# Kernel optimization log

Hardware: AMD Instinct MI355X
Metric: run time of the kernel (lower is better)

## Reference

```python
import jax, jax.numpy as jnp
import numpy as np

N, EMB, ATT = 65536, 1024, 512


def setup_inputs() -> dict:
    key = jax.random.key(0)
    k = jax.random.split(key, 6)
    scale = 0.02
    return {
        "leaves": jax.random.normal(k[0], (N, EMB), dtype=jnp.float32),
        "ancestors": jax.random.normal(k[1], (N, EMB), dtype=jnp.float32),
        "W1": jax.random.normal(k[2], (2 * EMB, ATT), dtype=jnp.float32) * scale,
        "b1": jax.random.normal(k[3], (ATT,), dtype=jnp.float32) * scale,
        "W2": jax.random.normal(k[4], (ATT, 1), dtype=jnp.float32) * scale,
        "b2": jax.random.normal(k[5], (1,), dtype=jnp.float32) * scale,
    }


def reference(leaves, ancestors, W1, b1, W2, b2):
    # concat -> [N, 2*EMB]
    x = jnp.concatenate([leaves, ancestors], axis=-1)
    # additive attention MLP: linear -> tanh -> linear -> [N, 1]
    h = jnp.tanh(x @ W1 + b1)
    scores = h @ W2 + b2            # [N, 1]
    attn = jax.nn.softmax(scores, axis=0)  # softmax over the pair dim
    # reshape to [1, N], matmul ancestors [N, EMB] -> [1, EMB], sum dim 0 -> [EMB]
    out = jnp.squeeze(attn, axis=1) @ ancestors  # [EMB]
    return out
```

## Files before the change

### kernel.cpp

```cpp
#include <hip/hip_runtime.h>
#include <hip/hip_bf16.h>
#include <stdint.h>
#include <stddef.h>

typedef __bf16 bf16;
typedef bf16 bf16x8 __attribute__((ext_vector_type(8)));
typedef float f32x4 __attribute__((ext_vector_type(4)));

#define N_ROWS 65536
#define EMB    1024
#define ATTD   512
#define KDIM   2048
#define BM     128
#define BN     128
#define BK     64
#define NKB    (KDIM / BK)
#define MBLK   (N_ROWS / BM)
#define NSPL   (ATTD / BN)

__device__ __forceinline__ void gload_lds16(const void* g, void* l) {
  __builtin_amdgcn_global_load_lds(
      (const __attribute__((address_space(1))) void*)g,
      (__attribute__((address_space(3))) void*)l, 16, 0, 0);
}

__global__ __launch_bounds__(256) void k_prep_w1(const float* __restrict__ W1,
                                                 bf16* __restrict__ W1t) {
  __shared__ float tile[64][132];
  const int kb = blockIdx.x;
  const int bn = blockIdx.y;
  const int t  = threadIdx.x;

  const int kr = t >> 2;
  const int nc = (t & 3) * 32;
  const float* src = W1 + (size_t)(kb * 64 + kr) * ATTD + bn * 128 + nc;
  #pragma unroll
  for (int q = 0; q < 8; ++q) {
    float4 v = *(const float4*)(src + q * 4);
    tile[kr][nc + q * 4 + 0] = v.x;
    tile[kr][nc + q * 4 + 1] = v.y;
    tile[kr][nc + q * 4 + 2] = v.z;
    tile[kr][nc + q * 4 + 3] = v.w;
  }
  __syncthreads();

  const int nl = t >> 1;
  const int pb = (t & 1) * 4;
  bf16* dst = W1t + (size_t)(kb * 4 + bn) * (BN * BK);
  #pragma unroll
  for (int pi = 0; pi < 4; ++pi) {
    const int p = pb + pi;
    const int c = p ^ (nl & 7);
    bf16x8 o;
    #pragma unroll
    for (int e = 0; e < 8; ++e) o[e] = (bf16)tile[c * 8 + e][nl];
    *(bf16x8*)(dst + ((size_t)nl * 8 + p) * 8) = o;
  }
}

__global__ __launch_bounds__(256, 3) void k_gemm_score(
    const float* __restrict__ leaves, const float* __restrict__ anc,
    const bf16* __restrict__ W1t, const float* __restrict__ b1,
    const float* __restrict__ W2, float* __restrict__ spart) {
  __shared__ float ldsAf[BM * BK];
  __shared__ bf16  ldsB[BN * BK];

  const int t    = threadIdx.x;
  const int lane = t & 63;
  const int wave = t >> 6;
  const int l15  = lane & 15;
  const int l4   = lane >> 4;
  const int wm2  = wave >> 1;
  const int wn2  = wave & 1;

  const int g   = blockIdx.x;
  const int sb  = g >> 5;
  const int q   = g & 31;
  const int bn  = q >> 3;
  const int bm  = sb * 8 + (q & 7);
  const int m0  = bm * BM;
  const int n0  = bn * BN;

  const int a_rbase = t >> 4;
  const int a_koff  = ((t & 15) ^ ((t >> 4) & 7)) * 4;

  const f32x4 zero4 = {0.f, 0.f, 0.f, 0.f};
  f32x4 acc[4][4];
  #pragma unroll
  for (int i = 0; i < 4; ++i)
    #pragma unroll
    for (int j = 0; j < 4; ++j) acc[i][j] = zero4;

  int a_rd_lo[2][4], a_rd_hi[2][4], b_rd[2][4];
  #pragma unroll
  for (int ks = 0; ks < 2; ++ks) {
    #pragma unroll
    for (int mi = 0; mi < 4; ++mi) {
      const int row = wm2 * 64 + mi * 16 + l15;
      const int c   = ks * 4 + l4;
      const int s3  = row & 7;
      a_rd_lo[ks][mi] = row * BK + ((2 * c)     ^ s3) * 4;
      a_rd_hi[ks][mi] = row * BK + ((2 * c + 1) ^ s3) * 4;
    }
    #pragma unroll
    for (int ni = 0; ni < 4; ++ni) {
      const int nrow = wn2 * 64 + ni * 16 + l15;
      b_rd[ks][ni] = nrow * BK + ((ks * 4 + l4) ^ (nrow & 7)) * 8;
    }
  }

  for (int kb = 0; kb < NKB; ++kb) {
    const bf16* Bsrc = W1t + (size_t)(kb * 4 + bn) * (BN * BK);
    #pragma unroll
    for (int j = 0; j < 4; ++j)
      gload_lds16(Bsrc + ((size_t)(wave * 4 + j) * 64 + lane) * 8,
                  ldsB + (wave * 4 + j) * 512);
    const float* Abase = (kb < 16)
        ? leaves + (size_t)m0 * EMB + (size_t)kb * BK
        : anc    + (size_t)m0 * EMB + (size_t)(kb - 16) * BK;
    #pragma unroll
    for (int s = 0; s < 8; ++s) {
      const int r = s * 16 + a_rbase;
      gload_lds16(Abase + (size_t)r * EMB + a_koff,
                  ldsAf + (s * 256 + t) * 4);
    }
    __syncthreads();
    #pragma unroll
    for (int ks = 0; ks < 2; ++ks) {
      bf16x8 af[4], bfr[4];
      #pragma unroll
      for (int mi = 0; mi < 4; ++mi) {
        f32x4 lo = *(const f32x4*)(ldsAf + a_rd_lo[ks][mi]);
        f32x4 hi = *(const f32x4*)(ldsAf + a_rd_hi[ks][mi]);
        af[mi] = (bf16x8){(bf16)lo.x, (bf16)lo.y, (bf16)lo.z, (bf16)lo.w,
                          (bf16)hi.x, (bf16)hi.y, (bf16)hi.z, (bf16)hi.w};
      }
      #pragma unroll
      for (int ni = 0; ni < 4; ++ni)
        bfr[ni] = *(const bf16x8*)(ldsB + b_rd[ks][ni]);
      #pragma unroll
      for (int ni = 0; ni < 4; ++ni)
        #pragma unroll
        for (int mi = 0; mi < 4; ++mi)
          acc[mi][ni] = __builtin_amdgcn_mfma_f32_16x16x32_bf16(
              af[mi], bfr[ni], acc[mi][ni], 0, 0, 0);
    }
    __syncthreads();
  }

  float b1c[4], w2c[4];
  #pragma unroll
  for (int ni = 0; ni < 4; ++ni) {
    const int col = n0 + wn2 * 64 + ni * 16 + l15;
    b1c[ni] = b1[col];
    w2c[ni] = W2[col];
  }
  float* sp = ldsAf;
  #pragma unroll
  for (int mi = 0; mi < 4; ++mi) {
    #pragma unroll
    for (int r = 0; r < 4; ++r) {
      float p = 0.f;
      #pragma unroll
      for (int ni = 0; ni < 4; ++ni)
        p += tanhf(acc[mi][ni][r] + b1c[ni]) * w2c[ni];
      p += __shfl_xor(p, 1);
      p += __shfl_xor(p, 2);
      p += __shfl_xor(p, 4);
      p += __shfl_xor(p, 8);
      if (l15 == 0) sp[wn2 * 128 + wm2 * 64 + mi * 16 + l4 * 4 + r] = p;
    }
  }
  __syncthreads();
  if (t < BM)
    spart[(size_t)bn * N_ROWS + m0 + t] = sp[t] + sp[128 + t];
}

__global__ __launch_bounds__(128) void k_combine(
    const float* __restrict__ spart, const float* __restrict__ b2,
    float* __restrict__ scores, float* __restrict__ bmax,
    float* __restrict__ bsum) {
  const int b = blockIdx.x, t = threadIdx.x;
  const int lane = t & 63, wave = t >> 6;
  const int m = b * 128 + t;
  __shared__ float rm[2], rs[2];
  const float s = spart[m] + spart[N_ROWS + m] + spart[2 * N_ROWS + m] +
                  spart[3 * N_ROWS + m] + b2[0];
  scores[m] = s;
  float mm = s;
  #pragma unroll
  for (int o = 32; o; o >>= 1) mm = fmaxf(mm, __shfl_xor(mm, o));
  if (lane == 0) rm[wave] = mm;
  __syncthreads();
  const float bM = fmaxf(rm[0], rm[1]);
  float ee = __expf(s - bM);
  #pragma unroll
  for (int o = 32; o; o >>= 1) ee += __shfl_xor(ee, o);
  if (lane == 0) rs[wave] = ee;
  __syncthreads();
  if (t == 0) {
    bmax[b] = bM;
    bsum[b] = rs[0] + rs[1];
  }
}

__global__ __launch_bounds__(512) void k_mz(const float* __restrict__ bmax,
                                            const float* __restrict__ bsum,
                                            float* __restrict__ MZ,
                                            float* __restrict__ scale) {
  const int t = threadIdx.x, lane = t & 63, wave = t >> 6;
  __shared__ float rm[8], rs[8];
  const float m = bmax[t];
  float mm = m;
  #pragma unroll
  for (int o = 32; o; o >>= 1) mm = fmaxf(mm, __shfl_xor(mm, o));
  if (lane == 0) rm[wave] = mm;
  __syncthreads();
  if (t == 0) {
    float g = rm[0];
    for (int i = 1; i < 8; ++i) g = fmaxf(g, rm[i]);
    rm[0] = g;
  }
  __syncthreads();
  const float M = rm[0];
  const float sc = __expf(m - M);
  scale[t] = sc;
  float z = bsum[t] * sc;
  #pragma unroll
  for (int o = 32; o; o >>= 1) z += __shfl_xor(z, o);
  if (lane == 0) rs[wave] = z;
  __syncthreads();
  if (t == 0) {
    float Z = 0.f;
    for (int i = 0; i < 8; ++i) Z += rs[i];
    MZ[0] = M;
    MZ[1] = Z;
  }
}

__global__ __launch_bounds__(256) void k_part(const float* __restrict__ anc,
                                              const float* __restrict__ scores,
                                              const float* __restrict__ bmax,
                                              float* __restrict__ part) {
  __shared__ float w[BM];
  const int b = blockIdx.x, t = threadIdx.x;
  const float bM = bmax[b];
  if (t < BM) w[t] = __expf(scores[(size_t)b * BM + t] - bM);
  __syncthreads();
  float4 a = {0.f, 0.f, 0.f, 0.f};
  const float4* src = (const float4*)(anc + (size_t)b * BM * EMB) + t;
  #pragma unroll 4
  for (int i = 0; i < BM; ++i) {
    float4 v = src[i * (EMB / 4)];
    const float wi = w[i];
    a.x += wi * v.x;
    a.y += wi * v.y;
    a.z += wi * v.z;
    a.w += wi * v.w;
  }
  ((float4*)(part + (size_t)b * EMB))[t] = a;
}

__global__ __launch_bounds__(256) void k_final(const float* __restrict__ part,
                                               const float* __restrict__ scale,
                                               const float* __restrict__ MZ,
                                               float* __restrict__ out) {
  const int j = blockIdx.x * 256 + threadIdx.x;
  float s0 = 0.f, s1 = 0.f, s2 = 0.f, s3 = 0.f;
  for (int b = 0; b < MBLK; b += 4) {
    s0 += part[(size_t)(b + 0) * EMB + j] * scale[b + 0];
    s1 += part[(size_t)(b + 1) * EMB + j] * scale[b + 1];
    s2 += part[(size_t)(b + 2) * EMB + j] * scale[b + 2];
    s3 += part[(size_t)(b + 3) * EMB + j] * scale[b + 3];
  }
  out[j] = (s0 + s1 + s2 + s3) / MZ[1];
}

extern "C" void kernel_launch(void* const* d_in, const int* in_sizes, int n_in,
                              void* d_out, int out_size, void* d_ws,
                              size_t ws_size, hipStream_t stream) {
  const float* leaves = (const float*)d_in[0];
  const float* anc    = (const float*)d_in[1];
  const float* W1     = (const float*)d_in[2];
  const float* b1     = (const float*)d_in[3];
  const float* W2     = (const float*)d_in[4];
  const float* b2     = (const float*)d_in[5];
  float* out = (float*)d_out;

  char* ws = (char*)d_ws;
  bf16*  W1t    = (bf16*)ws;
  float* spart  = (float*)(ws + (2u << 20));
  float* scores = (float*)(ws + (3u << 20));
  float* bmax   = (float*)(ws + (3u << 20) + (1u << 18));
  float* bsum   = bmax + MBLK;
  float* scale  = bsum + MBLK;
  float* MZ     = scale + MBLK;
  float* part   = (float*)(ws + (4u << 20));

  k_prep_w1<<<dim3(32, 4), 256, 0, stream>>>(W1, W1t);
  k_gemm_score<<<dim3(MBLK * NSPL), 256, 0, stream>>>(leaves, anc, W1t, b1, W2,
                                                      spart);
  k_combine<<<dim3(MBLK), 128, 0, stream>>>(spart, b2, scores, bmax, bsum);
  k_mz<<<dim3(1), 512, 0, stream>>>(bmax, bsum, MZ, scale);
  k_part<<<dim3(MBLK), 256, 0, stream>>>(anc, scores, bmax, part);
  k_final<<<dim3(EMB / 256), 256, 0, stream>>>(part, scale, MZ, out);
}
```

Baseline: 291.8 us.

## Load W1 fragments directly into registers with double-buffered prefetch, drop B LDS

```diff
diff --git a/kernel.cpp b/kernel.cpp
--- a/kernel.cpp
+++ b/kernel.cpp
@@ -44,17 +44,18 @@
   }
   __syncthreads();
 
-  const int nl = t >> 1;
+  const int n  = t >> 1;
   const int pb = (t & 1) * 4;
   bf16* dst = W1t + (size_t)(kb * 4 + bn) * (BN * BK);
   #pragma unroll
   for (int pi = 0; pi < 4; ++pi) {
-    const int p = pb + pi;
-    const int c = p ^ (nl & 7);
+    const int c    = pb + pi;
+    const int frag = (((n >> 6) * 4) + ((n >> 4) & 3)) * 2 + (c >> 2);
+    const int lane = (c & 3) * 16 + (n & 15);
     bf16x8 o;
     #pragma unroll
-    for (int e = 0; e < 8; ++e) o[e] = (bf16)tile[c * 8 + e][nl];
-    *(bf16x8*)(dst + ((size_t)nl * 8 + p) * 8) = o;
+    for (int e = 0; e < 8; ++e) o[e] = (bf16)tile[c * 8 + e][n];
+    *(bf16x8*)(dst + frag * 512 + lane * 8) = o;
   }
 }
 
@@ -63,7 +64,6 @@
     const bf16* __restrict__ W1t, const float* __restrict__ b1,
     const float* __restrict__ W2, float* __restrict__ spart) {
   __shared__ float ldsAf[BM * BK];
-  __shared__ bf16  ldsB[BN * BK];
 
   const int t    = threadIdx.x;
   const int lane = t & 63;
@@ -84,14 +84,7 @@
   const int a_rbase = t >> 4;
   const int a_koff  = ((t & 15) ^ ((t >> 4) & 7)) * 4;
 
-  const f32x4 zero4 = {0.f, 0.f, 0.f, 0.f};
-  f32x4 acc[4][4];
-  #pragma unroll
-  for (int i = 0; i < 4; ++i)
-    #pragma unroll
-    for (int j = 0; j < 4; ++j) acc[i][j] = zero4;
-
-  int a_rd_lo[2][4], a_rd_hi[2][4], b_rd[2][4];
+  int a_rd_lo[2][4], a_rd_hi[2][4];
   #pragma unroll
   for (int ks = 0; ks < 2; ++ks) {
     #pragma unroll
@@ -102,51 +95,78 @@
       a_rd_lo[ks][mi] = row * BK + ((2 * c)     ^ s3) * 4;
       a_rd_hi[ks][mi] = row * BK + ((2 * c + 1) ^ s3) * 4;
     }
+  }
+
+  const f32x4 zero4 = {0.f, 0.f, 0.f, 0.f};
+  f32x4 acc[4][4];
+  #pragma unroll
+  for (int i = 0; i < 4; ++i)
     #pragma unroll
-    for (int ni = 0; ni < 4; ++ni) {
-      const int nrow = wn2 * 64 + ni * 16 + l15;
-      b_rd[ks][ni] = nrow * BK + ((ks * 4 + l4) ^ (nrow & 7)) * 8;
-    }
-  }
-
-  for (int kb = 0; kb < NKB; ++kb) {
-    const bf16* Bsrc = W1t + (size_t)(kb * 4 + bn) * (BN * BK);
-    #pragma unroll
-    for (int j = 0; j < 4; ++j)
-      gload_lds16(Bsrc + ((size_t)(wave * 4 + j) * 64 + lane) * 8,
-                  ldsB + (wave * 4 + j) * 512);
-    const float* Abase = (kb < 16)
-        ? leaves + (size_t)m0 * EMB + (size_t)kb * BK
-        : anc    + (size_t)m0 * EMB + (size_t)(kb - 16) * BK;
-    #pragma unroll
-    for (int s = 0; s < 8; ++s) {
-      const int r = s * 16 + a_rbase;
-      gload_lds16(Abase + (size_t)r * EMB + a_koff,
-                  ldsAf + (s * 256 + t) * 4);
-    }
+    for (int j = 0; j < 4; ++j) acc[i][j] = zero4;
+
+  const bf16* Bbase = W1t + (size_t)bn * (BN * BK) + (wn2 * 8) * 512 + lane * 8;
+  bf16x8 B0[8], B1[8];
+
+#define LOADB(KB, BARR)                                                        \
+  do {                                                                         \
+    const bf16* bp_ = Bbase + (size_t)(KB) * (4 * BN * BK);                    \
+    _Pragma("unroll")                                                          \
+    for (int f_ = 0; f_ < 8; ++f_)                                             \
+      BARR[f_] = *(const bf16x8*)(bp_ + f_ * 512);                             \
+  } while (0)
+
+#define ISSUE_A(KB)                                                            \
+  do {                                                                         \
+    const float* Abase_ = ((KB) < 16)                                          \
+        ? leaves + (size_t)m0 * EMB + (size_t)(KB)*BK                          \
+        : anc    + (size_t)m0 * EMB + (size_t)((KB) - 16) * BK;                \
+    _Pragma("unroll")                                                          \
+    for (int s_ = 0; s_ < 8; ++s_) {                                           \
+      const int r_ = s_ * 16 + a_rbase;                                        \
+      gload_lds16(Abase_ + (size_t)r_ * EMB + a_koff,                          \
+                  ldsAf + (s_ * 256 + t) * 4);                                 \
+    }                                                                          \
+  } while (0)
+
+#define COMPUTE(BARR)                                                          \
+  do {                                                                         \
+    _Pragma("unroll")                                                          \
+    for (int ks = 0; ks < 2; ++ks) {                                           \
+      bf16x8 af[4];                                                            \
+      _Pragma("unroll")                                                        \
+      for (int mi = 0; mi < 4; ++mi) {                                         \
+        f32x4 lo = *(const f32x4*)(ldsAf + a_rd_lo[ks][mi]);                   \
+        f32x4 hi = *(const f32x4*)(ldsAf + a_rd_hi[ks][mi]);                   \
+        af[mi] = (bf16x8){(bf16)lo.x, (bf16)lo.y, (bf16)lo.z, (bf16)lo.w,      \
+                          (bf16)hi.x, (bf16)hi.y, (bf16)hi.z, (bf16)hi.w};     \
+      }                                                                        \
+      _Pragma("unroll")                                                        \
+      for (int ni = 0; ni < 4; ++ni)                                           \
+        _Pragma("unroll")                                                      \
+        for (int mi = 0; mi < 4; ++mi)                                         \
+          acc[mi][ni] = __builtin_amdgcn_mfma_f32_16x16x32_bf16(               \
+              af[mi], BARR[ni * 2 + ks], acc[mi][ni], 0, 0, 0);                \
+    }                                                                          \
+  } while (0)
+
+  LOADB(0, B0);
+
+  for (int kbp = 0; kbp < NKB / 2; ++kbp) {
+    const int kb = 2 * kbp;
+    ISSUE_A(kb);
+    if (kb + 1 < NKB) LOADB(kb + 1, B1);
     __syncthreads();
-    #pragma unroll
-    for (int ks = 0; ks < 2; ++ks) {
-      bf16x8 af[4], bfr[4];
-      #pragma unroll
-      for (int mi = 0; mi < 4; ++mi) {
-        f32x4 lo = *(const f32x4*)(ldsAf + a_rd_lo[ks][mi]);
-        f32x4 hi = *(const f32x4*)(ldsAf + a_rd_hi[ks][mi]);
-        af[mi] = (bf16x8){(bf16)lo.x, (bf16)lo.y, (bf16)lo.z, (bf16)lo.w,
-                          (bf16)hi.x, (bf16)hi.y, (bf16)hi.z, (bf16)hi.w};
-      }
-      #pragma unroll
-      for (int ni = 0; ni < 4; ++ni)
-        bfr[ni] = *(const bf16x8*)(ldsB + b_rd[ks][ni]);
-      #pragma unroll
-      for (int ni = 0; ni < 4; ++ni)
-        #pragma unroll
-        for (int mi = 0; mi < 4; ++mi)
-          acc[mi][ni] = __builtin_amdgcn_mfma_f32_16x16x32_bf16(
-              af[mi], bfr[ni], acc[mi][ni], 0, 0, 0);
-    }
+    COMPUTE(B0);
     __syncthreads();
-  }
+    ISSUE_A(kb + 1);
+    if (kb + 2 < NKB) LOADB(kb + 2, B0);
+    __syncthreads();
+    COMPUTE(B1);
+    __syncthreads();
+  }
+#undef LOADB
+#undef ISSUE_A
+#undef COMPUTE
 
   float b1c[4], w2c[4];
   #pragma unroll
```

Measured after the change: 562.9 us. +92.9%, slower.

## Pre-swizzle W1 into MFMA fragment order and load B directly to registers

Applied to the files above, without the earlier changes.

```diff
diff --git a/kernel.cpp b/kernel.cpp
--- a/kernel.cpp
+++ b/kernel.cpp
@@ -44,17 +44,18 @@
   }
   __syncthreads();
 
-  const int nl = t >> 1;
+  const int n  = t >> 1;
   const int pb = (t & 1) * 4;
   bf16* dst = W1t + (size_t)(kb * 4 + bn) * (BN * BK);
   #pragma unroll
   for (int pi = 0; pi < 4; ++pi) {
-    const int p = pb + pi;
-    const int c = p ^ (nl & 7);
+    const int c    = pb + pi;
+    const int frag = (((n >> 6) * 4) + ((n >> 4) & 3)) * 2 + (c >> 2);
+    const int lane = (c & 3) * 16 + (n & 15);
     bf16x8 o;
     #pragma unroll
-    for (int e = 0; e < 8; ++e) o[e] = (bf16)tile[c * 8 + e][nl];
-    *(bf16x8*)(dst + ((size_t)nl * 8 + p) * 8) = o;
+    for (int e = 0; e < 8; ++e) o[e] = (bf16)tile[c * 8 + e][n];
+    *(bf16x8*)(dst + frag * 512 + lane * 8) = o;
   }
 }
 
@@ -63,7 +64,6 @@
     const bf16* __restrict__ W1t, const float* __restrict__ b1,
     const float* __restrict__ W2, float* __restrict__ spart) {
   __shared__ float ldsAf[BM * BK];
-  __shared__ bf16  ldsB[BN * BK];
 
   const int t    = threadIdx.x;
   const int lane = t & 63;
@@ -84,14 +84,7 @@
   const int a_rbase = t >> 4;
   const int a_koff  = ((t & 15) ^ ((t >> 4) & 7)) * 4;
 
-  const f32x4 zero4 = {0.f, 0.f, 0.f, 0.f};
-  f32x4 acc[4][4];
-  #pragma unroll
-  for (int i = 0; i < 4; ++i)
-    #pragma unroll
-    for (int j = 0; j < 4; ++j) acc[i][j] = zero4;
-
-  int a_rd_lo[2][4], a_rd_hi[2][4], b_rd[2][4];
+  int a_rd_lo[2][4], a_rd_hi[2][4];
   #pragma unroll
   for (int ks = 0; ks < 2; ++ks) {
     #pragma unroll
@@ -102,19 +95,18 @@
       a_rd_lo[ks][mi] = row * BK + ((2 * c)     ^ s3) * 4;
       a_rd_hi[ks][mi] = row * BK + ((2 * c + 1) ^ s3) * 4;
     }
-    #pragma unroll
-    for (int ni = 0; ni < 4; ++ni) {
-      const int nrow = wn2 * 64 + ni * 16 + l15;
-      b_rd[ks][ni] = nrow * BK + ((ks * 4 + l4) ^ (nrow & 7)) * 8;
-    }
-  }
+  }
+
+  const f32x4 zero4 = {0.f, 0.f, 0.f, 0.f};
+  f32x4 acc[4][4];
+  #pragma unroll
+  for (int i = 0; i < 4; ++i)
+    #pragma unroll
+    for (int j = 0; j < 4; ++j) acc[i][j] = zero4;
+
+  const bf16* Bbase = W1t + (size_t)bn * (BN * BK) + (wn2 * 8) * 512 + lane * 8;
 
   for (int kb = 0; kb < NKB; ++kb) {
-    const bf16* Bsrc = W1t + (size_t)(kb * 4 + bn) * (BN * BK);
-    #pragma unroll
-    for (int j = 0; j < 4; ++j)
-      gload_lds16(Bsrc + ((size_t)(wave * 4 + j) * 64 + lane) * 8,
-                  ldsB + (wave * 4 + j) * 512);
     const float* Abase = (kb < 16)
         ? leaves + (size_t)m0 * EMB + (size_t)kb * BK
         : anc    + (size_t)m0 * EMB + (size_t)(kb - 16) * BK;
@@ -124,10 +116,17 @@
       gload_lds16(Abase + (size_t)r * EMB + a_koff,
                   ldsAf + (s * 256 + t) * 4);
     }
+    bf16x8 B[8];
+    {
+      const bf16* bp = Bbase + (size_t)kb * (4 * BN * BK);
+      #pragma unroll
+      for (int f = 0; f < 8; ++f)
+        B[f] = *(const bf16x8*)(bp + f * 512);
+    }
     __syncthreads();
     #pragma unroll
     for (int ks = 0; ks < 2; ++ks) {
-      bf16x8 af[4], bfr[4];
+      bf16x8 af[4];
       #pragma unroll
       for (int mi = 0; mi < 4; ++mi) {
         f32x4 lo = *(const f32x4*)(ldsAf + a_rd_lo[ks][mi]);
@@ -137,13 +136,10 @@
       }
       #pragma unroll
       for (int ni = 0; ni < 4; ++ni)
-        bfr[ni] = *(const bf16x8*)(ldsB + b_rd[ks][ni]);
-      #pragma unroll
-      for (int ni = 0; ni < 4; ++ni)
         #pragma unroll
         for (int mi = 0; mi < 4; ++mi)
           acc[mi][ni] = __builtin_amdgcn_mfma_f32_16x16x32_bf16(
-              af[mi], bfr[ni], acc[mi][ni], 0, 0, 0);
+              af[mi], B[ni * 2 + ks], acc[mi][ni], 0, 0, 0);
     }
     __syncthreads();
   }
```

After: 306.6 us. +5.1%, slower.
